# Performance work log

Measured on AMD Instinct MI355X. Metric: run time of the kernel, lower is better.

The kernel has to match this reference:

```python
import jax, jax.numpy as jnp
import numpy as np

N_SPARSE = 2  # keep N of every M weights (2:4 structured sparsity)
M_SPARSE = 4


def compute_mask(w, n, m):
    # w: [out, in]; zero the (m - n) smallest-|w| entries in each group of m
    out_f, in_f = w.shape
    k = m - n
    wr = jnp.abs(w).reshape(out_f, in_f // m, m)
    # indices of the k smallest |w| per group (torch.topk largest=False)
    _, idx = jax.lax.top_k(-wr, k)                      # [out, in/m, k]
    pruned = jax.nn.one_hot(idx, m, dtype=w.dtype).sum(axis=-2)  # [out, in/m, m]
    mask = 1.0 - pruned
    return mask.reshape(out_f, in_f)


def setup_inputs() -> dict:
    key = jax.random.key(0)
    k1, k2, k3 = jax.random.split(key, 3)
    B, S, Din, Dout = 64, 197, 768, 3072
    x = jax.random.normal(k1, (B, S, Din), dtype=jnp.float32)
    weight = jax.random.normal(k2, (Dout, Din), dtype=jnp.float32)
    bias = jax.random.normal(k3, (Dout,), dtype=jnp.float32)
    return {"x": x, "weight": weight, "bias": bias}


def reference(x, weight, bias):
    # mask is a precomputed buffer in torch (not differentiated)
    mask = compute_mask(jax.lax.stop_gradient(weight), N_SPARSE, M_SPARSE)
    w = weight * mask
    # F.linear: x @ w.T + b
    return jnp.einsum('bsi,oi->bso', x, w) + bias
```

## Files before the change

### kernel.cpp

```cpp
#include <hip/hip_runtime.h>
#include <hip/hip_bf16.h>

#define M_DIM 12608
#define K_DIM 768
#define N_DIM 3072
#define M_PAD 12672
#define BM 128
#define BN 128
#define BK 64

typedef __attribute__((ext_vector_type(8))) short bf16x8;
typedef __attribute__((ext_vector_type(4))) float f32x4;

__device__ __forceinline__ void gload_lds16(const void* g, void* l) {
  __builtin_amdgcn_global_load_lds(
      (const __attribute__((address_space(1))) unsigned int*)g,
      (__attribute__((address_space(3))) unsigned int*)l,
      16, 0, 0);
}

__global__ void cvt_x(const float* __restrict__ x, __hip_bfloat16* __restrict__ xb) {
  size_t i = ((size_t)blockIdx.x * blockDim.x + threadIdx.x) * 8;
  if (i >= (size_t)M_PAD * K_DIM) return;
  union { __hip_bfloat16 h[8]; uint4 u; } o;
  if (i < (size_t)M_DIM * K_DIM) {
    float4 a = *(const float4*)(x + i);
    float4 b = *(const float4*)(x + i + 4);
    o.h[0] = __float2bfloat16(a.x); o.h[1] = __float2bfloat16(a.y);
    o.h[2] = __float2bfloat16(a.z); o.h[3] = __float2bfloat16(a.w);
    o.h[4] = __float2bfloat16(b.x); o.h[5] = __float2bfloat16(b.y);
    o.h[6] = __float2bfloat16(b.z); o.h[7] = __float2bfloat16(b.w);
  } else {
    o.u = make_uint4(0, 0, 0, 0);
  }
  *(uint4*)(xb + i) = o.u;
}

__global__ void cvt_w(const float* __restrict__ w, __hip_bfloat16* __restrict__ wb) {
  size_t g = (size_t)blockIdx.x * blockDim.x + threadIdx.x;
  if (g >= (size_t)N_DIM * (K_DIM / 4)) return;
  float4 v = *(const float4*)(w + g * 4);
  float val[4] = {v.x, v.y, v.z, v.w};
  float a[4] = {fabsf(v.x), fabsf(v.y), fabsf(v.z), fabsf(v.w)};
  union { __hip_bfloat16 h[4]; uint2 u; } o;
#pragma unroll
  for (int i = 0; i < 4; ++i) {
    int rank = 0;
#pragma unroll
    for (int j = 0; j < 4; ++j)
      rank += (a[j] > a[i]) || (a[j] == a[i] && j > i);
    o.h[i] = __float2bfloat16(rank < 2 ? val[i] : 0.0f);
  }
  *(uint2*)(wb + g * 4) = o.u;
}

__global__ __launch_bounds__(256) void gemm_bt(
    const __hip_bfloat16* __restrict__ A,
    const __hip_bfloat16* __restrict__ B,
    const float* __restrict__ bias,
    float* __restrict__ C)
{
  __shared__ __hip_bfloat16 As[BM * BK];
  __shared__ __hip_bfloat16 Bs[BN * BK];

  const int tid  = threadIdx.x;
  const int lane = tid & 63;
  const int wave = tid >> 6;
  const int wm = wave >> 1, wn = wave & 1;

  const int tile_m = blockIdx.y * BM;
  const int tile_n = blockIdx.x * BN;

  const int lrow = lane >> 3;
  const int lcol = (lane & 7) * 8;

  const int frow = lane & 15;
  const int fcol = (lane >> 4) * 8;

  f32x4 acc[4][4] = {};

  for (int k0 = 0; k0 < K_DIM; k0 += BK) {
    __syncthreads();
#pragma unroll
    for (int i = 0; i < 4; ++i) {
      const int seg = wave * 4 + i;
      gload_lds16(A + (size_t)(tile_m + seg * 8 + lrow) * K_DIM + k0 + lcol,
                  &As[seg * 8 * BK]);
    }
#pragma unroll
    for (int i = 0; i < 4; ++i) {
      const int seg = wave * 4 + i;
      gload_lds16(B + (size_t)(tile_n + seg * 8 + lrow) * K_DIM + k0 + lcol,
                  &Bs[seg * 8 * BK]);
    }
    __syncthreads();

#pragma unroll
    for (int kk = 0; kk < BK; kk += 32) {
      bf16x8 af[4], bfr[4];
#pragma unroll
      for (int i = 0; i < 4; ++i)
        af[i] = *(const bf16x8*)&As[(wm * 64 + i * 16 + frow) * BK + kk + fcol];
#pragma unroll
      for (int j = 0; j < 4; ++j)
        bfr[j] = *(const bf16x8*)&Bs[(wn * 64 + j * 16 + frow) * BK + kk + fcol];
#pragma unroll
      for (int i = 0; i < 4; ++i)
#pragma unroll
        for (int j = 0; j < 4; ++j)
          acc[i][j] = __builtin_amdgcn_mfma_f32_16x16x32_bf16(af[i], bfr[j], acc[i][j], 0, 0, 0);
    }
  }

  const int quad = lane >> 4;
  const int ccol = lane & 15;
#pragma unroll
  for (int j = 0; j < 4; ++j) {
    const int gcol = tile_n + wn * 64 + j * 16 + ccol;
    const float bv = bias[gcol];
#pragma unroll
    for (int i = 0; i < 4; ++i) {
      const int rbase = tile_m + wm * 64 + i * 16 + quad * 4;
#pragma unroll
      for (int r = 0; r < 4; ++r) {
        const int grow = rbase + r;
        if (grow < M_DIM)
          C[(size_t)grow * N_DIM + gcol] = acc[i][j][r] + bv;
      }
    }
  }
}

extern "C" void kernel_launch(void* const* d_in, const int* in_sizes, int n_in,
                              void* d_out, int out_size, void* d_ws, size_t ws_size,
                              hipStream_t stream) {
  const float* x    = (const float*)d_in[0];
  const float* w    = (const float*)d_in[1];
  const float* bias = (const float*)d_in[2];
  float* out = (float*)d_out;

  __hip_bfloat16* xb = (__hip_bfloat16*)d_ws;
  __hip_bfloat16* wb = xb + (size_t)M_PAD * K_DIM;

  cvt_x<<<(M_PAD * K_DIM / 8 + 255) / 256, 256, 0, stream>>>(x, xb);
  cvt_w<<<(N_DIM * (K_DIM / 4) + 255) / 256, 256, 0, stream>>>(w, wb);

  dim3 grid(N_DIM / BN, M_PAD / BM);
  gemm_bt<<<grid, 256, 0, stream>>>(xb, wb, bias, out);
}
```

Baseline: 306.1 us.

## Double-buffer LDS tiles with XOR swizzle and stage epilogue through LDS

```diff
diff --git a/kernel.cpp b/kernel.cpp
--- a/kernel.cpp
+++ b/kernel.cpp
@@ -7,7 +7,7 @@
 #define M_PAD 12672
 #define BM 128
 #define BN 128
-#define BK 64
+#define BK 32
 
 typedef __attribute__((ext_vector_type(8))) short bf16x8;
 typedef __attribute__((ext_vector_type(4))) float f32x4;
@@ -60,8 +60,7 @@
     const float* __restrict__ bias,
     float* __restrict__ C)
 {
-  __shared__ __hip_bfloat16 As[BM * BK];
-  __shared__ __hip_bfloat16 Bs[BN * BK];
+  __shared__ char smem[32768];
 
   const int tid  = threadIdx.x;
   const int lane = tid & 63;
@@ -71,62 +70,91 @@
   const int tile_m = blockIdx.y * BM;
   const int tile_n = blockIdx.x * BN;
 
-  const int lrow = lane >> 3;
-  const int lcol = (lane & 7) * 8;
+  const int ris  = lane >> 2;
+  const int slot = lane & 3;
+  const int arow0 = wave * 32 + ris;
+  const int arow1 = arow0 + 16;
+  const int acg0 = slot ^ (arow0 & 3) ^ ((arow0 >> 2) & 3);
+  const int acg1 = slot ^ (arow1 & 3) ^ ((arow1 >> 2) & 3);
+  const __hip_bfloat16* ag0 = A + (size_t)(tile_m + arow0) * K_DIM + acg0 * 8;
+  const __hip_bfloat16* ag1 = A + (size_t)(tile_m + arow1) * K_DIM + acg1 * 8;
+  const __hip_bfloat16* bg0 = B + (size_t)(tile_n + arow0) * K_DIM + acg0 * 8;
+  const __hip_bfloat16* bg1 = B + (size_t)(tile_n + arow1) * K_DIM + acg1 * 8;
 
-  const int frow = lane & 15;
-  const int fcol = (lane >> 4) * 8;
+  const int frow  = lane & 15;
+  const int fslot = (lane >> 4) ^ (lane & 3) ^ ((lane & 15) >> 2);
+  const int aoff = (wm * 64 + frow) * 64 + fslot * 16;
+  const int boff = (wn * 64 + frow) * 64 + fslot * 16;
 
   f32x4 acc[4][4] = {};
 
-  for (int k0 = 0; k0 < K_DIM; k0 += BK) {
+  {
+    char* ba = smem + wave * 2048;
+    char* bb = smem + 8192 + wave * 2048;
+    gload_lds16(ag0, ba);
+    gload_lds16(ag1, ba + 1024);
+    gload_lds16(bg0, bb);
+    gload_lds16(bg1, bb + 1024);
+  }
+
+  const int NITER = K_DIM / BK;
+  for (int k = 0; k < NITER; ++k) {
+    const int cur = k & 1;
+    __syncthreads();
+
+    if (k + 1 < NITER) {
+      const int off = (k + 1) * BK;
+      char* ba = smem + (cur ^ 1) * 16384 + wave * 2048;
+      char* bb = smem + (cur ^ 1) * 16384 + 8192 + wave * 2048;
+      gload_lds16(ag0 + off, ba);
+      gload_lds16(ag1 + off, ba + 1024);
+      gload_lds16(bg0 + off, bb);
+      gload_lds16(bg1 + off, bb + 1024);
+    }
+
+    const char* sa = smem + cur * 16384;
+    const char* sb = sa + 8192;
+    bf16x8 af[4], bfr[4];
+#pragma unroll
+    for (int i = 0; i < 4; ++i)
+      af[i] = *(const bf16x8*)(sa + aoff + i * 1024);
+#pragma unroll
+    for (int j = 0; j < 4; ++j)
+      bfr[j] = *(const bf16x8*)(sb + boff + j * 1024);
+#pragma unroll
+    for (int i = 0; i < 4; ++i)
+#pragma unroll
+      for (int j = 0; j < 4; ++j)
+        acc[i][j] = __builtin_amdgcn_mfma_f32_16x16x32_bf16(af[i], bfr[j], acc[i][j], 0, 0, 0);
+  }
+
+  const int ccol = lane & 15;
+  const int quad = lane >> 4;
+  float bv[4];
+#pragma unroll
+  for (int j = 0; j < 4; ++j)
+    bv[j] = bias[tile_n + wn * 64 + j * 16 + ccol];
+
+  float* tr = (float*)smem + wave * 1088;
+  const int erow = lane >> 2;
+  const int eseg = lane & 3;
+
+  #pragma unroll
+  for (int i = 0; i < 4; ++i) {
     __syncthreads();
 #pragma unroll
-    for (int i = 0; i < 4; ++i) {
-      const int seg = wave * 4 + i;
-      gload_lds16(A + (size_t)(tile_m + seg * 8 + lrow) * K_DIM + k0 + lcol,
-                  &As[seg * 8 * BK]);
-    }
+    for (int j = 0; j < 4; ++j)
 #pragma unroll
-    for (int i = 0; i < 4; ++i) {
-      const int seg = wave * 4 + i;
-      gload_lds16(B + (size_t)(tile_n + seg * 8 + lrow) * K_DIM + k0 + lcol,
-                  &Bs[seg * 8 * BK]);
-    }
+      for (int r = 0; r < 4; ++r)
+        tr[(quad * 4 + r) * 68 + j * 16 + ccol] = acc[i][j][r] + bv[j];
     __syncthreads();
-
+    const int grow = tile_m + wm * 64 + i * 16 + erow;
+    if (grow < M_DIM) {
+      float* dst = C + (size_t)grow * N_DIM + tile_n + wn * 64 + eseg * 16;
+      const float* src = tr + erow * 68 + eseg * 16;
 #pragma unroll
-    for (int kk = 0; kk < BK; kk += 32) {
-      bf16x8 af[4], bfr[4];
-#pragma unroll
-      for (int i = 0; i < 4; ++i)
-        af[i] = *(const bf16x8*)&As[(wm * 64 + i * 16 + frow) * BK + kk + fcol];
-#pragma unroll
-      for (int j = 0; j < 4; ++j)
-        bfr[j] = *(const bf16x8*)&Bs[(wn * 64 + j * 16 + frow) * BK + kk + fcol];
-#pragma unroll
-      for (int i = 0; i < 4; ++i)
-#pragma unroll
-        for (int j = 0; j < 4; ++j)
-          acc[i][j] = __builtin_amdgcn_mfma_f32_16x16x32_bf16(af[i], bfr[j], acc[i][j], 0, 0, 0);
-    }
-  }
-
-  const int quad = lane >> 4;
-  const int ccol = lane & 15;
-#pragma unroll
-  for (int j = 0; j < 4; ++j) {
-    const int gcol = tile_n + wn * 64 + j * 16 + ccol;
-    const float bv = bias[gcol];
-#pragma unroll
-    for (int i = 0; i < 4; ++i) {
-      const int rbase = tile_m + wm * 64 + i * 16 + quad * 4;
-#pragma unroll
-      for (int r = 0; r < 4; ++r) {
-        const int grow = rbase + r;
-        if (grow < M_DIM)
-          C[(size_t)grow * N_DIM + gcol] = acc[i][j][r] + bv;
-      }
+      for (int u = 0; u < 4; ++u)
+        *(f32x4*)(dst + u * 4) = *(const f32x4*)(src + u * 4);
     }
   }
 }
```

Measured after the change: 278.6 us. 9.0% less time.
